# Kernel tuning notes

Measured on AMD Instinct MI355X. Metric: run time of the kernel, lower is better.

The kernel has to match this reference:

```python
import jax, jax.numpy as jnp
import numpy as np

N_NODES = 10000
N_EDGES = 640000
IN_CH = 128
OUT_CH = 128


def setup_inputs() -> dict:
    key = jax.random.key(0)
    k1, k2, k3, k4 = jax.random.split(key, 4)
    x = jax.random.normal(k1, (N_NODES, IN_CH), dtype=jnp.float32)
    edge_index = jax.random.randint(k2, (2, N_EDGES), 0, N_NODES, dtype=jnp.int64)
    # nn.Linear(2*in_channels, out_channels): weight [out, 2*in], bias [out]
    bound = 1.0 / np.sqrt(2 * IN_CH)
    W = jax.random.uniform(k3, (OUT_CH, 2 * IN_CH), dtype=jnp.float32, minval=-bound, maxval=bound)
    b = jax.random.uniform(k4, (OUT_CH,), dtype=jnp.float32, minval=-bound, maxval=bound)
    return {"x": x, "W": W, "b": b, "edge_index": edge_index}


def reference(x, W, b, edge_index):
    # PyG convention: edge_index[0] = source j, edge_index[1] = target i
    src, dst = edge_index[0], edge_index[1]
    x_i = x[dst]                      # [E, C] target features
    x_j = x[src]                      # [E, C] source features
    feat = jnp.concatenate([x_i, x_j - x_i], axis=-1)  # [E, 2C]
    msg = feat @ W.T + b              # [E, out]
    out = jax.ops.segment_max(msg, dst, num_segments=x.shape[0])  # [N, out]
    # isolated nodes: PyG scatter-max yields 0, segment_max yields -inf
    return jnp.where(jnp.isfinite(out), out, 0.0)
```

## Files before the change

kernel.cpp:

```cpp
#include <hip/hip_runtime.h>
#include <math.h>

#define N_CH 128
#define NB_MAX 512
#define BIN_CHUNK 4096
#define BIN_T 512

__global__ __launch_bounds__(256) void prep_kernel(const float* __restrict__ W,
                                                   float* __restrict__ V1,
                                                   float* __restrict__ V2,
                                                   int* __restrict__ binCount,
                                                   int nb) {
    int i = blockIdx.x * 256 + threadIdx.x;
    if (i < N_CH * N_CH) {
        int k = i >> 7, o = i & 127;
        float w1 = W[o * 256 + k];
        float w2 = W[o * 256 + 128 + k];
        V1[i] = w1 - w2;
        V2[i] = w2;
    }
    if (i < nb) binCount[i] = 0;
}

__global__ __launch_bounds__(256) void gemm_kernel(const float* __restrict__ x,
                                                   const float* __restrict__ V1,
                                                   const float* __restrict__ V2,
                                                   float* __restrict__ A,
                                                   float* __restrict__ Bm,
                                                   int n_nodes) {
    __shared__ float xs[32][N_CH];
    const int n0 = blockIdx.x * 32;
    const int tid = threadIdx.x;

    if (n0 + 32 <= n_nodes) {
        const float4* xg = (const float4*)(x + (size_t)n0 * N_CH);
        float4* xsv = (float4*)&xs[0][0];
        #pragma unroll
        for (int i = 0; i < 4; ++i) xsv[tid + i * 256] = xg[tid + i * 256];
    } else {
        for (int i = tid; i < 32 * N_CH; i += 256) {
            int n = n0 + (i >> 7);
            (&xs[0][0])[i] = (n < n_nodes) ? x[(size_t)n * N_CH + (i & 127)] : 0.f;
        }
    }
    __syncthreads();

    const int o  = tid & 127;
    const int nh = tid >> 7;
    float acc1[16], acc2[16];
    #pragma unroll
    for (int i = 0; i < 16; ++i) { acc1[i] = 0.f; acc2[i] = 0.f; }

    const float* xrow = &xs[nh * 16][0];
    for (int k4 = 0; k4 < N_CH; k4 += 4) {
        float w1[4], w2[4];
        #pragma unroll
        for (int j = 0; j < 4; ++j) {
            w1[j] = V1[(k4 + j) * N_CH + o];
            w2[j] = V2[(k4 + j) * N_CH + o];
        }
        #pragma unroll
        for (int i = 0; i < 16; ++i) {
            float4 xv = *(const float4*)&xrow[i * N_CH + k4];
            acc1[i] = fmaf(xv.x, w1[0], acc1[i]); acc2[i] = fmaf(xv.x, w2[0], acc2[i]);
            acc1[i] = fmaf(xv.y, w1[1], acc1[i]); acc2[i] = fmaf(xv.y, w2[1], acc2[i]);
            acc1[i] = fmaf(xv.z, w1[2], acc1[i]); acc2[i] = fmaf(xv.z, w2[2], acc2[i]);
            acc1[i] = fmaf(xv.w, w1[3], acc1[i]); acc2[i] = fmaf(xv.w, w2[3], acc2[i]);
        }
    }

    #pragma unroll
    for (int i = 0; i < 16; ++i) {
        int n = n0 + nh * 16 + i;
        if (n < n_nodes) {
            A [(size_t)n * N_CH + o] = acc1[i];
            Bm[(size_t)n * N_CH + o] = acc2[i];
        }
    }
}

__global__ __launch_bounds__(256) void bhist_kernel(const int* __restrict__ dst,
                                                    int* __restrict__ binCount,
                                                    int n_edges, int nb) {
    __shared__ int h[NB_MAX];
    const int tid = threadIdx.x;
    for (int i = tid; i < nb; i += 256) h[i] = 0;
    __syncthreads();
    const int base = blockIdx.x * BIN_CHUNK;
    const int cnt = min(BIN_CHUNK, n_edges - base);
    for (int j = tid; j < cnt; j += 256)
        atomicAdd(&h[dst[base + j] >> 5], 1);
    __syncthreads();
    for (int i = tid; i < nb; i += 256)
        if (h[i]) atomicAdd(&binCount[i], h[i]);
}

__global__ __launch_bounds__(512) void bscan_kernel(const int* __restrict__ binCount,
                                                    int* __restrict__ binOff,
                                                    int* __restrict__ binCursor,
                                                    int nb) {
    __shared__ int t[512];
    const int tid = threadIdx.x;
    int v = (tid < nb) ? binCount[tid] : 0;
    t[tid] = v;
    __syncthreads();
    #pragma unroll
    for (int off = 1; off < 512; off <<= 1) {
        int u = (tid >= off) ? t[tid - off] : 0;
        __syncthreads();
        t[tid] += u;
        __syncthreads();
    }
    if (tid < nb) {
        int excl = t[tid] - v;
        binOff[tid] = excl;
        binCursor[tid] = excl;
    }
    if (tid == 0) binOff[nb] = t[nb - 1];
}

__global__ __launch_bounds__(BIN_T) void bin_kernel(const int* __restrict__ src,
                                                    const int* __restrict__ dst,
                                                    int* __restrict__ binCursor,
                                                    unsigned int* __restrict__ binned,
                                                    int n_edges, int nb) {
    __shared__ unsigned int   lpk[BIN_CHUNK];
    __shared__ unsigned short lbk[BIN_CHUNK];
    __shared__ int sc[512];
    __shared__ int lhist[NB_MAX], lexcl[NB_MAX], lcur[NB_MAX], bbase[NB_MAX];

    const int tid = threadIdx.x;
    const int base = blockIdx.x * BIN_CHUNK;
    const int cnt = min(BIN_CHUNK, n_edges - base);

    for (int i = tid; i < nb; i += BIN_T) lhist[i] = 0;
    __syncthreads();

    unsigned int vreg[BIN_CHUNK / BIN_T];
    unsigned short breg[BIN_CHUNK / BIN_T];
    int nloc = 0;
    for (int j = tid; j < cnt; j += BIN_T) {
        int s = src[base + j];
        int d = dst[base + j];
        int b = d >> 5;
        vreg[nloc] = ((unsigned int)(d & 31) << 14) | (unsigned int)s;
        breg[nloc] = (unsigned short)b;
        ++nloc;
        atomicAdd(&lhist[b], 1);
    }
    __syncthreads();

    int v = (tid < nb) ? lhist[tid] : 0;
    sc[tid] = v;
    __syncthreads();
    #pragma unroll
    for (int off = 1; off < 512; off <<= 1) {
        int u = (tid >= off) ? sc[tid - off] : 0;
        __syncthreads();
        sc[tid] += u;
        __syncthreads();
    }
    if (tid < nb) {
        int excl = sc[tid] - v;
        lexcl[tid] = excl;
        lcur[tid] = excl;
    }
    __syncthreads();

    for (int k = 0; k < nloc; ++k) {
        int b = breg[k];
        int p = atomicAdd(&lcur[b], 1);
        lpk[p] = vreg[k];
        lbk[p] = (unsigned short)b;
    }
    __syncthreads();

    for (int b = tid; b < nb; b += BIN_T) {
        int c = lhist[b];
        if (c) bbase[b] = atomicAdd(&binCursor[b], c);
    }
    __syncthreads();

    for (int i = tid; i < cnt; i += BIN_T) {
        int b = lbk[i];
        binned[bbase[b] + (i - lexcl[b])] = lpk[i];
    }
}

__global__ __launch_bounds__(256) void build_kernel(const unsigned int* __restrict__ binned,
                                                    const int* __restrict__ binOff,
                                                    int* __restrict__ offsets,
                                                    int* __restrict__ eidx,
                                                    int n_nodes, int nb) {
    __shared__ int lhist[32], lexcl[33], lcur[32];
    const int b = blockIdx.x;
    const int tid = threadIdx.x;
    const int rbeg = binOff[b], rend = binOff[b + 1];

    if (tid < 32) { lhist[tid] = 0; lcur[tid] = 0; }
    __syncthreads();
    for (int i = rbeg + tid; i < rend; i += 256)
        atomicAdd(&lhist[binned[i] >> 14], 1);
    __syncthreads();
    if (tid == 0) {
        int s = 0;
        for (int k = 0; k < 32; ++k) { lexcl[k] = s; s += lhist[k]; }
        lexcl[32] = s;
    }
    __syncthreads();
    if (tid < 32) {
        int n = b * 32 + tid;
        if (n < n_nodes) offsets[n] = rbeg + lexcl[tid];
    }
    if (b == nb - 1 && tid == 0) offsets[n_nodes] = rend;
    for (int i = rbeg + tid; i < rend; i += 256) {
        unsigned int w = binned[i];
        int d5 = (int)(w >> 14);
        int r = atomicAdd(&lcur[d5], 1);
        eidx[rbeg + lexcl[d5] + r] = (int)(w & 16383u);
    }
}

__global__ __launch_bounds__(128) void gather_kernel(const float* __restrict__ A,
                                                     const float* __restrict__ Bm,
                                                     const float* __restrict__ b,
                                                     const int* __restrict__ offsets,
                                                     const int* __restrict__ eidx,
                                                     float* __restrict__ out,
                                                     int n_nodes) {
    __shared__ int sidx[128];
    const int n = blockIdx.x;
    const int c = threadIdx.x;
    const int beg = offsets[n], end = offsets[n + 1];

    float m[8];
    #pragma unroll
    for (int i = 0; i < 8; ++i) m[i] = -INFINITY;

    for (int base = beg; base < end; base += 128) {
        int p = base + c;
        if (p < end) sidx[c] = eidx[p];
        __syncthreads();
        int cnt = min(128, end - base);
        int q = 0;
        for (; q + 8 <= cnt; q += 8) {
            #pragma unroll
            for (int i = 0; i < 8; ++i)
                m[i] = fmaxf(m[i], Bm[(size_t)sidx[q + i] * N_CH + c]);
        }
        for (; q < cnt; ++q)
            m[0] = fmaxf(m[0], Bm[(size_t)sidx[q] * N_CH + c]);
        __syncthreads();
    }
    float mm = fmaxf(fmaxf(fmaxf(m[0], m[1]), fmaxf(m[2], m[3])),
                     fmaxf(fmaxf(m[4], m[5]), fmaxf(m[6], m[7])));
    float r = (end > beg) ? (A[(size_t)n * N_CH + c] + b[c] + mm) : 0.f;
    out[(size_t)n * N_CH + c] = r;
}

extern "C" void kernel_launch(void* const* d_in, const int* in_sizes, int n_in,
                              void* d_out, int out_size, void* d_ws, size_t ws_size,
                              hipStream_t stream) {
    const float* x = (const float*)d_in[0];
    const float* W = (const float*)d_in[1];
    const float* b = (const float*)d_in[2];
    const int*   ei = (const int*)d_in[3];

    const int n_nodes = in_sizes[0] / N_CH;
    const int n_edges = in_sizes[3] / 2;
    const int nb = (n_nodes + 31) >> 5;
    const int* src = ei;
    const int* dst = ei + n_edges;
    float* out = (float*)d_out;

    char* ws = (char*)d_ws;
    size_t off = 0;
    auto alloc = [&](size_t bytes) -> void* {
        void* p = ws + off;
        off += (bytes + 255) & ~(size_t)255;
        return p;
    };
    float* V1        = (float*)alloc((size_t)N_CH * N_CH * 4);
    float* V2        = (float*)alloc((size_t)N_CH * N_CH * 4);
    float* A         = (float*)alloc((size_t)n_nodes * N_CH * 4);
    float* Bm        = (float*)alloc((size_t)n_nodes * N_CH * 4);
    int*   binCount  = (int*)alloc((size_t)nb * 4);
    int*   binOff    = (int*)alloc((size_t)(nb + 1) * 4);
    int*   binCursor = (int*)alloc((size_t)nb * 4);
    unsigned int* binned = (unsigned int*)alloc((size_t)n_edges * 4);
    int*   offsets   = (int*)alloc((size_t)(n_nodes + 1) * 4);
    int*   eidx      = (int*)alloc((size_t)n_edges * 4);
    (void)ws_size; (void)n_in; (void)out_size;

    const int nbin_blocks = (n_edges + BIN_CHUNK - 1) / BIN_CHUNK;

    prep_kernel <<<(N_CH * N_CH + 255) / 256, 256, 0, stream>>>(W, V1, V2, binCount, nb);
    gemm_kernel <<<(n_nodes + 31) / 32, 256, 0, stream>>>(x, V1, V2, A, Bm, n_nodes);
    bhist_kernel<<<nbin_blocks, 256, 0, stream>>>(dst, binCount, n_edges, nb);
    bscan_kernel<<<1, 512, 0, stream>>>(binCount, binOff, binCursor, nb);
    bin_kernel  <<<nbin_blocks, BIN_T, 0, stream>>>(src, dst, binCursor, binned, n_edges, nb);
    build_kernel<<<nb, 256, 0, stream>>>(binned, binOff, offsets, eidx, n_nodes, nb);
    gather_kernel<<<n_nodes, 128, 0, stream>>>(A, Bm, b, offsets, eidx, out, n_nodes);
}
```

Measured before the change: 143.9 us.

## Fuse CSR build and gather into per-bin bucket max with bf16 source table

Replaces the build and per-node gather kernels with one kernel per 32-node bin. Each bin sorts its edges by target in shared memory, gathers source rows from a bf16-rounded table, and reduces with ordered-key atomicMax into a shared accumulator. Bias is folded into the A term in the GEMM epilogue. This removes one launch, the eidx/offsets round trip, and half the gather bytes. In exchange it adds bf16 rounding error to the max values and shared-memory atomics.

```diff
diff --git a/kernel.cpp b/kernel.cpp
--- a/kernel.cpp
+++ b/kernel.cpp
@@ -5,6 +5,18 @@
 #define NB_MAX 512
 #define BIN_CHUNK 4096
 #define BIN_T 512
+#define BM_T 512
+#define BM_CAP 4096
+
+__device__ inline unsigned int fkey(float f) {
+    unsigned int b = __float_as_uint(f);
+    return (b & 0x80000000u) ? ~b : (b | 0x80000000u);
+}
+__device__ inline float keyf(unsigned int k) {
+    unsigned int b = (k & 0x80000000u) ? (k & 0x7FFFFFFFu) : ~k;
+    return __uint_as_float(b);
+}
+#define NEG_INF_KEY 0x007FFFFFu
 
 __global__ __launch_bounds__(256) void prep_kernel(const float* __restrict__ W,
                                                    float* __restrict__ V1,
@@ -25,8 +37,9 @@
 __global__ __launch_bounds__(256) void gemm_kernel(const float* __restrict__ x,
                                                    const float* __restrict__ V1,
                                                    const float* __restrict__ V2,
+                                                   const float* __restrict__ bias,
                                                    float* __restrict__ A,
-                                                   float* __restrict__ Bm,
+                                                   unsigned short* __restrict__ Bh,
                                                    int n_nodes) {
     __shared__ float xs[32][N_CH];
     const int n0 = blockIdx.x * 32;
@@ -47,6 +60,7 @@
 
     const int o  = tid & 127;
     const int nh = tid >> 7;
+    const float bo = bias[o];
     float acc1[16], acc2[16];
     #pragma unroll
     for (int i = 0; i < 16; ++i) { acc1[i] = 0.f; acc2[i] = 0.f; }
@@ -73,8 +87,10 @@
     for (int i = 0; i < 16; ++i) {
         int n = n0 + nh * 16 + i;
         if (n < n_nodes) {
-            A [(size_t)n * N_CH + o] = acc1[i];
-            Bm[(size_t)n * N_CH + o] = acc2[i];
+            A[(size_t)n * N_CH + o] = acc1[i] + bo;
+            unsigned int bits = __float_as_uint(acc2[i]);
+            unsigned int r = (bits + 0x7FFFu + ((bits >> 16) & 1u)) >> 16;
+            Bh[(size_t)n * N_CH + o] = (unsigned short)r;
         }
     }
 }
@@ -187,75 +203,83 @@
     }
 }
 
-__global__ __launch_bounds__(256) void build_kernel(const unsigned int* __restrict__ binned,
-                                                    const int* __restrict__ binOff,
-                                                    int* __restrict__ offsets,
-                                                    int* __restrict__ eidx,
-                                                    int n_nodes, int nb) {
-    __shared__ int lhist[32], lexcl[33], lcur[32];
+__global__ __launch_bounds__(BM_T) void bucketmax_kernel(
+        const unsigned int* __restrict__ binned,
+        const int* __restrict__ binOff,
+        const float* __restrict__ A,
+        const unsigned short* __restrict__ Bh,
+        float* __restrict__ out,
+        int n_nodes) {
+    __shared__ unsigned int sidx[BM_CAP];
+    __shared__ unsigned int accU[32 * N_CH];
+    __shared__ int lhist[32], lexcl[32], lcur[32];
+
     const int b = blockIdx.x;
     const int tid = threadIdx.x;
     const int rbeg = binOff[b], rend = binOff[b + 1];
 
-    if (tid < 32) { lhist[tid] = 0; lcur[tid] = 0; }
-    __syncthreads();
-    for (int i = rbeg + tid; i < rend; i += 256)
-        atomicAdd(&lhist[binned[i] >> 14], 1);
-    __syncthreads();
-    if (tid == 0) {
-        int s = 0;
-        for (int k = 0; k < 32; ++k) { lexcl[k] = s; s += lhist[k]; }
-        lexcl[32] = s;
-    }
-    __syncthreads();
-    if (tid < 32) {
-        int n = b * 32 + tid;
-        if (n < n_nodes) offsets[n] = rbeg + lexcl[tid];
-    }
-    if (b == nb - 1 && tid == 0) offsets[n_nodes] = rend;
-    for (int i = rbeg + tid; i < rend; i += 256) {
-        unsigned int w = binned[i];
-        int d5 = (int)(w >> 14);
-        int r = atomicAdd(&lcur[d5], 1);
-        eidx[rbeg + lexcl[d5] + r] = (int)(w & 16383u);
-    }
-}
-
-__global__ __launch_bounds__(128) void gather_kernel(const float* __restrict__ A,
-                                                     const float* __restrict__ Bm,
-                                                     const float* __restrict__ b,
-                                                     const int* __restrict__ offsets,
-                                                     const int* __restrict__ eidx,
-                                                     float* __restrict__ out,
-                                                     int n_nodes) {
-    __shared__ int sidx[128];
-    const int n = blockIdx.x;
-    const int c = threadIdx.x;
-    const int beg = offsets[n], end = offsets[n + 1];
-
-    float m[8];
-    #pragma unroll
-    for (int i = 0; i < 8; ++i) m[i] = -INFINITY;
-
-    for (int base = beg; base < end; base += 128) {
-        int p = base + c;
-        if (p < end) sidx[c] = eidx[p];
-        __syncthreads();
-        int cnt = min(128, end - base);
-        int q = 0;
-        for (; q + 8 <= cnt; q += 8) {
+    for (int i = tid; i < 32 * N_CH; i += BM_T) accU[i] = NEG_INF_KEY;
+
+    for (int cbeg = rbeg; cbeg < rend; cbeg += BM_CAP) {
+        const int cnt = min(BM_CAP, rend - cbeg);
+        if (tid < 32) lhist[tid] = 0;
+        __syncthreads();
+        for (int j = tid; j < cnt; j += BM_T)
+            atomicAdd(&lhist[binned[cbeg + j] >> 14], 1);
+        __syncthreads();
+        if (tid == 0) {
+            int s = 0;
             #pragma unroll
-            for (int i = 0; i < 8; ++i)
-                m[i] = fmaxf(m[i], Bm[(size_t)sidx[q + i] * N_CH + c]);
-        }
-        for (; q < cnt; ++q)
-            m[0] = fmaxf(m[0], Bm[(size_t)sidx[q] * N_CH + c]);
-        __syncthreads();
-    }
-    float mm = fmaxf(fmaxf(fmaxf(m[0], m[1]), fmaxf(m[2], m[3])),
-                     fmaxf(fmaxf(m[4], m[5]), fmaxf(m[6], m[7])));
-    float r = (end > beg) ? (A[(size_t)n * N_CH + c] + b[c] + mm) : 0.f;
-    out[(size_t)n * N_CH + c] = r;
+            for (int k = 0; k < 32; ++k) { lexcl[k] = s; lcur[k] = s; s += lhist[k]; }
+        }
+        __syncthreads();
+        for (int j = tid; j < cnt; j += BM_T) {
+            unsigned int w = binned[cbeg + j];
+            int p = atomicAdd(&lcur[w >> 14], 1);
+            sidx[p] = w;
+        }
+        __syncthreads();
+
+        const int g  = tid >> 7;
+        const int gc = tid & 127;
+        const int per = (cnt + 3) >> 2;
+        const int gb = g * per;
+        const int ge = min(cnt, gb + per);
+        float run = -INFINITY;
+        int cur = -1;
+        for (int i = gb; i < ge; i += 4) {
+            const int lim = min(4, ge - i);
+            unsigned int w[4];
+            float v[4];
+            for (int j = 0; j < lim; ++j) w[j] = sidx[i + j];
+            for (int j = 0; j < lim; ++j) {
+                unsigned short h = Bh[(size_t)(w[j] & 16383u) * N_CH + gc];
+                v[j] = __uint_as_float((unsigned int)h << 16);
+            }
+            for (int j = 0; j < lim; ++j) {
+                int d5 = (int)(w[j] >> 14);
+                if (d5 != cur) {
+                    if (cur >= 0) atomicMax(&accU[cur * N_CH + gc], fkey(run));
+                    cur = d5;
+                    run = -INFINITY;
+                }
+                run = fmaxf(run, v[j]);
+            }
+        }
+        if (cur >= 0) atomicMax(&accU[cur * N_CH + gc], fkey(run));
+        __syncthreads();
+    }
+
+    for (int i = tid; i < 32 * N_CH; i += BM_T) {
+        int node = b * 32 + (i >> 7);
+        if (node < n_nodes) {
+            unsigned int k = accU[i];
+            float r = 0.f;
+            if (k != NEG_INF_KEY)
+                r = A[(size_t)node * N_CH + (i & 127)] + keyf(k);
+            out[(size_t)node * N_CH + (i & 127)] = r;
+        }
+    }
 }
 
 extern "C" void kernel_launch(void* const* d_in, const int* in_sizes, int n_in,
@@ -283,22 +307,19 @@
     float* V1        = (float*)alloc((size_t)N_CH * N_CH * 4);
     float* V2        = (float*)alloc((size_t)N_CH * N_CH * 4);
     float* A         = (float*)alloc((size_t)n_nodes * N_CH * 4);
-    float* Bm        = (float*)alloc((size_t)n_nodes * N_CH * 4);
+    unsigned short* Bh = (unsigned short*)alloc((size_t)n_nodes * N_CH * 2);
     int*   binCount  = (int*)alloc((size_t)nb * 4);
     int*   binOff    = (int*)alloc((size_t)(nb + 1) * 4);
     int*   binCursor = (int*)alloc((size_t)nb * 4);
     unsigned int* binned = (unsigned int*)alloc((size_t)n_edges * 4);
-    int*   offsets   = (int*)alloc((size_t)(n_nodes + 1) * 4);
-    int*   eidx      = (int*)alloc((size_t)n_edges * 4);
     (void)ws_size; (void)n_in; (void)out_size;
 
     const int nbin_blocks = (n_edges + BIN_CHUNK - 1) / BIN_CHUNK;
 
     prep_kernel <<<(N_CH * N_CH + 255) / 256, 256, 0, stream>>>(W, V1, V2, binCount, nb);
-    gemm_kernel <<<(n_nodes + 31) / 32, 256, 0, stream>>>(x, V1, V2, A, Bm, n_nodes);
+    gemm_kernel <<<(n_nodes + 31) / 32, 256, 0, stream>>>(x, V1, V2, b, A, Bh, n_nodes);
     bhist_kernel<<<nbin_blocks, 256, 0, stream>>>(dst, binCount, n_edges, nb);
     bscan_kernel<<<1, 512, 0, stream>>>(binCount, binOff, binCursor, nb);
     bin_kernel  <<<nbin_blocks, BIN_T, 0, stream>>>(src, dst, binCursor, binned, n_edges, nb);
-    build_kernel<<<nb, 256, 0, stream>>>(binned, binOff, offsets, eidx, n_nodes, nb);
-    gather_kernel<<<n_nodes, 128, 0, stream>>>(A, Bm, b, offsets, eidx, out, n_nodes);
-}
+    bucketmax_kernel<<<nb, BM_T, 0, stream>>>(binned, binOff, A, Bh, out, n_nodes);
+}
```

New measurement: 368.6 us. +156.2%, slower.

## Store source projection in bf16 and gather with one wavefront per node

Applied to the files above, without the earlier changes.

The per-node source projection Bm is rounded to bf16 in the GEMM epilogue, and the bias is folded into A there as well. The gather kernel now uses one 64-lane wavefront per node, packing four nodes per block, and each lane reads two bf16 channels as one 32-bit word. This drops the block-level syncs and halves the bytes read by the random-access gather, which is the bandwidth-bound stage. The cost is bf16 rounding of the messages before the max, which may exceed tolerance. The shared index buffer is also now reused across iterations without a barrier, relying on wavefront lockstep.

```diff
diff --git a/kernel.cpp b/kernel.cpp
--- a/kernel.cpp
+++ b/kernel.cpp
@@ -25,8 +25,9 @@
 __global__ __launch_bounds__(256) void gemm_kernel(const float* __restrict__ x,
                                                    const float* __restrict__ V1,
                                                    const float* __restrict__ V2,
+                                                   const float* __restrict__ bias,
                                                    float* __restrict__ A,
-                                                   float* __restrict__ Bm,
+                                                   unsigned short* __restrict__ Bh,
                                                    int n_nodes) {
     __shared__ float xs[32][N_CH];
     const int n0 = blockIdx.x * 32;
@@ -47,6 +48,7 @@
 
     const int o  = tid & 127;
     const int nh = tid >> 7;
+    const float bo = bias[o];
     float acc1[16], acc2[16];
     #pragma unroll
     for (int i = 0; i < 16; ++i) { acc1[i] = 0.f; acc2[i] = 0.f; }
@@ -73,8 +75,10 @@
     for (int i = 0; i < 16; ++i) {
         int n = n0 + nh * 16 + i;
         if (n < n_nodes) {
-            A [(size_t)n * N_CH + o] = acc1[i];
-            Bm[(size_t)n * N_CH + o] = acc2[i];
+            A[(size_t)n * N_CH + o] = acc1[i] + bo;
+            unsigned int bits = __float_as_uint(acc2[i]);
+            unsigned int r = (bits + 0x7FFFu + ((bits >> 16) & 1u)) >> 16;
+            Bh[(size_t)n * N_CH + o] = (unsigned short)r;
         }
     }
 }
@@ -221,41 +225,58 @@
     }
 }
 
-__global__ __launch_bounds__(128) void gather_kernel(const float* __restrict__ A,
-                                                     const float* __restrict__ Bm,
-                                                     const float* __restrict__ b,
-                                                     const int* __restrict__ offsets,
-                                                     const int* __restrict__ eidx,
-                                                     float* __restrict__ out,
-                                                     int n_nodes) {
-    __shared__ int sidx[128];
-    const int n = blockIdx.x;
-    const int c = threadIdx.x;
+__global__ __launch_bounds__(256) void gather_kernel(
+        const float* __restrict__ A,
+        const unsigned int* __restrict__ Bh2,
+        const int* __restrict__ offsets,
+        const int* __restrict__ eidx,
+        float* __restrict__ out,
+        int n_nodes) {
+    __shared__ int sidx[4][64];
+    const int g = threadIdx.x >> 6;
+    const int l = threadIdx.x & 63;
+    const int n = blockIdx.x * 4 + g;
+    if (n >= n_nodes) return;
     const int beg = offsets[n], end = offsets[n + 1];
 
-    float m[8];
-    #pragma unroll
-    for (int i = 0; i < 8; ++i) m[i] = -INFINITY;
-
-    for (int base = beg; base < end; base += 128) {
-        int p = base + c;
-        if (p < end) sidx[c] = eidx[p];
-        __syncthreads();
-        int cnt = min(128, end - base);
+    float mlo[8], mhi[8];
+    #pragma unroll
+    for (int i = 0; i < 8; ++i) { mlo[i] = -INFINITY; mhi[i] = -INFINITY; }
+
+    for (int base = beg; base < end; base += 64) {
+        int p = base + l;
+        if (p < end) sidx[g][l] = eidx[p];
+        int cnt = min(64, end - base);
         int q = 0;
         for (; q + 8 <= cnt; q += 8) {
+            unsigned int w[8];
             #pragma unroll
             for (int i = 0; i < 8; ++i)
-                m[i] = fmaxf(m[i], Bm[(size_t)sidx[q + i] * N_CH + c]);
-        }
-        for (; q < cnt; ++q)
-            m[0] = fmaxf(m[0], Bm[(size_t)sidx[q] * N_CH + c]);
-        __syncthreads();
-    }
-    float mm = fmaxf(fmaxf(fmaxf(m[0], m[1]), fmaxf(m[2], m[3])),
-                     fmaxf(fmaxf(m[4], m[5]), fmaxf(m[6], m[7])));
-    float r = (end > beg) ? (A[(size_t)n * N_CH + c] + b[c] + mm) : 0.f;
-    out[(size_t)n * N_CH + c] = r;
+                w[i] = Bh2[(size_t)sidx[g][q + i] * 64 + l];
+            #pragma unroll
+            for (int i = 0; i < 8; ++i) {
+                mlo[i] = fmaxf(mlo[i], __uint_as_float(w[i] << 16));
+                mhi[i] = fmaxf(mhi[i], __uint_as_float(w[i] & 0xFFFF0000u));
+            }
+        }
+        for (; q < cnt; ++q) {
+            unsigned int w = Bh2[(size_t)sidx[g][q] * 64 + l];
+            mlo[0] = fmaxf(mlo[0], __uint_as_float(w << 16));
+            mhi[0] = fmaxf(mhi[0], __uint_as_float(w & 0xFFFF0000u));
+        }
+    }
+
+    float lo = mlo[0], hi = mhi[0];
+    #pragma unroll
+    for (int i = 1; i < 8; ++i) { lo = fmaxf(lo, mlo[i]); hi = fmaxf(hi, mhi[i]); }
+
+    float2 r = make_float2(0.f, 0.f);
+    if (end > beg) {
+        float2 a = *(const float2*)(A + (size_t)n * N_CH + 2 * l);
+        r.x = a.x + lo;
+        r.y = a.y + hi;
+    }
+    *(float2*)(out + (size_t)n * N_CH + 2 * l) = r;
 }
 
 extern "C" void kernel_launch(void* const* d_in, const int* in_sizes, int n_in,
@@ -283,7 +304,7 @@
     float* V1        = (float*)alloc((size_t)N_CH * N_CH * 4);
     float* V2        = (float*)alloc((size_t)N_CH * N_CH * 4);
     float* A         = (float*)alloc((size_t)n_nodes * N_CH * 4);
-    float* Bm        = (float*)alloc((size_t)n_nodes * N_CH * 4);
+    unsigned short* Bh = (unsigned short*)alloc((size_t)n_nodes * N_CH * 2);
     int*   binCount  = (int*)alloc((size_t)nb * 4);
     int*   binOff    = (int*)alloc((size_t)(nb + 1) * 4);
     int*   binCursor = (int*)alloc((size_t)nb * 4);
@@ -295,10 +316,10 @@
     const int nbin_blocks = (n_edges + BIN_CHUNK - 1) / BIN_CHUNK;
 
     prep_kernel <<<(N_CH * N_CH + 255) / 256, 256, 0, stream>>>(W, V1, V2, binCount, nb);
-    gemm_kernel <<<(n_nodes + 31) / 32, 256, 0, stream>>>(x, V1, V2, A, Bm, n_nodes);
+    gemm_kernel <<<(n_nodes + 31) / 32, 256, 0, stream>>>(x, V1, V2, b, A, Bh, n_nodes);
     bhist_kernel<<<nbin_blocks, 256, 0, stream>>>(dst, binCount, n_edges, nb);
     bscan_kernel<<<1, 512, 0, stream>>>(binCount, binOff, binCursor, nb);
     bin_kernel  <<<nbin_blocks, BIN_T, 0, stream>>>(src, dst, binCursor, binned, n_edges, nb);
     build_kernel<<<nb, 256, 0, stream>>>(binned, binOff, offsets, eidx, n_nodes, nb);
-    gather_kernel<<<n_nodes, 128, 0, stream>>>(A, Bm, b, offsets, eidx, out, n_nodes);
-}
+    gather_kernel<<<(n_nodes + 3) / 4, 256, 0, stream>>>(A, (const unsigned int*)Bh, offsets, eidx, out, n_nodes);
+}
```

After: 138.5 us. 3.8% less time.
